# Optimization experiments

Measured on AMD Instinct MI355X. Metric: run time of the kernel, lower is better.

## Reference

```python
import jax, jax.numpy as jnp
import numpy as np

N_EMBD = 1024
N_HEAD = 16
HEAD_DIM = N_EMBD // N_HEAD
SCALE = HEAD_DIM ** -0.5


def setup_inputs() -> dict:
    key = jax.random.key(0)
    ks = jax.random.split(key, 6)
    B, T = 64, 256
    s = N_EMBD ** -0.5
    return {
        "x": jax.random.normal(ks[0], (B, T, N_EMBD), dtype=jnp.float32),
        "Wq": jax.random.normal(ks[1], (N_EMBD, N_EMBD), dtype=jnp.float32) * s,
        "Wk": jax.random.normal(ks[2], (N_EMBD, N_EMBD), dtype=jnp.float32) * s,
        "Wv": jax.random.normal(ks[3], (N_EMBD, N_EMBD), dtype=jnp.float32) * s,
        "Wo": jax.random.normal(ks[4], (N_EMBD, N_EMBD), dtype=jnp.float32) * s,
        "bo": jax.random.normal(ks[5], (N_EMBD,), dtype=jnp.float32) * 0.01,
    }


def reference(x, Wq, Wk, Wv, Wo, bo):
    B, T, C = x.shape
    # QKV projections (no bias), split heads -> [B, H, T, Dh]
    def heads(y):
        return y.reshape(B, T, N_HEAD, HEAD_DIM).transpose(0, 2, 1, 3)
    q = heads(x @ Wq)
    k = heads(x @ Wk)
    v = heads(x @ Wv)
    # scaled causal attention scores [B, H, T, T]
    wei = jnp.einsum("bhqd,bhkd->bhqk", q, k) * SCALE
    causal = jnp.tril(jnp.ones((T, T), dtype=bool))
    wei = jnp.where(causal, wei, -jnp.inf)
    wei = jax.nn.softmax(wei, axis=-1)
    # dropout is identity in eval mode
    out = jnp.einsum("bhqk,bhkd->bhqd", wei, v)
    out = out.transpose(0, 2, 1, 3).reshape(B, T, C)
    return out @ Wo + bo
```

## Files before the change

kernel.cpp:

```cpp
#include <hip/hip_runtime.h>
#include <hip/hip_bf16.h>
#include <stdint.h>

typedef __attribute__((ext_vector_type(8))) short bfx8;
typedef __attribute__((ext_vector_type(4))) short bfx4;
typedef __attribute__((ext_vector_type(4))) float f32x4;
typedef __attribute__((ext_vector_type(4))) unsigned short us4;

#define SCALE_ATT 0.125f

__device__ __forceinline__ unsigned short f2bf(float f) {
  union { float f; unsigned u; } a; a.f = f;
  unsigned r = a.u + 0x7fffu + ((a.u >> 16) & 1u);
  return (unsigned short)(r >> 16);
}

__device__ __forceinline__ void gll16(const void* g, void* l) {
  __builtin_amdgcn_global_load_lds(
      (__attribute__((address_space(1))) void*)(g),
      (__attribute__((address_space(3))) void*)(l), 16, 0, 0);
}

__device__ __forceinline__ bfx8 ld2x64(const unsigned short* p) {
  bfx4 lo = *(const bfx4*)p;
  bfx4 hi = *(const bfx4*)(p + 4);
  return __builtin_shufflevector(lo, hi, 0, 1, 2, 3, 4, 5, 6, 7);
}

__global__ __launch_bounds__(256) void cvt_x(const float* __restrict__ x,
                                             unsigned short* __restrict__ xb, int n4) {
  int i = blockIdx.x * blockDim.x + threadIdx.x;
  int stride = gridDim.x * blockDim.x;
  const float4* x4 = (const float4*)x;
  for (; i < n4; i += stride) {
    float4 v = x4[i];
    us4 o;
    o[0] = f2bf(v.x); o[1] = f2bf(v.y); o[2] = f2bf(v.z); o[3] = f2bf(v.w);
    *(us4*)&xb[(size_t)i * 4] = o;
  }
}

__global__ __launch_bounds__(256) void cvt_w(const float* __restrict__ W0, const float* __restrict__ W1,
                                             const float* __restrict__ W2, const float* __restrict__ W3,
                                             unsigned short* __restrict__ T0, unsigned short* __restrict__ T1,
                                             unsigned short* __restrict__ T2, unsigned short* __restrict__ T3) {
  const float* W; unsigned short* T;
  switch (blockIdx.z) {
    case 0: W = W0; T = T0; break;
    case 1: W = W1; T = T1; break;
    case 2: W = W2; T = T2; break;
    default: W = W3; T = T3; break;
  }
  __shared__ unsigned short Ts[64][68];
  int k0 = blockIdx.x * 64, n0 = blockIdx.y * 64;
  int t = threadIdx.x;
  int lrow = t >> 4, c4 = t & 15;
  #pragma unroll
  for (int i = 0; i < 4; i++) {
    int row = lrow + i * 16;
    float4 v = *(const float4*)&W[(size_t)(k0 + row) * 1024 + n0 + c4 * 4];
    Ts[c4 * 4 + 0][row] = f2bf(v.x);
    Ts[c4 * 4 + 1][row] = f2bf(v.y);
    Ts[c4 * 4 + 2][row] = f2bf(v.z);
    Ts[c4 * 4 + 3][row] = f2bf(v.w);
  }
  __syncthreads();
  #pragma unroll
  for (int i = 0; i < 4; i++) {
    int nrow = lrow + i * 16;
    us4 v = *(const us4*)&Ts[nrow][c4 * 4];
    *(us4*)&T[(size_t)(n0 + nrow) * 1024 + k0 + c4 * 4] = v;
  }
}

#define DS_BAR() __builtin_amdgcn_s_barrier()
#define LGKM0() do { asm volatile("s_waitcnt lgkmcnt(0)" ::: "memory"); \
                     __builtin_amdgcn_sched_barrier(0); } while (0)
#define VMW4() asm volatile("s_waitcnt vmcnt(4)" ::: "memory")
#define VMW0() asm volatile("s_waitcnt vmcnt(0)" ::: "memory")

#define STAGE(hs, gb, r0, kbyte) do { \
  const char* _g = (const char*)(gb) + (size_t)((r0) + srow) * 2048 + (size_t)(kbyte) + scolb; \
  gll16(_g, (hs) + w * 1024); \
  gll16(_g + 16 * 2048, (hs) + w * 1024 + 512); \
} while (0)

#define LOADA(dst, hs, qm) \
  _Pragma("unroll") for (int mi = 0; mi < 4; ++mi) \
    dst[mi] = *(const bfx8*)&(hs)[(wm * 128 + (qm) * 64 + mi * 16 + lr) * 32 + rcol];

#define LOADB(dst, hs) \
  _Pragma("unroll") for (int ni = 0; ni < 4; ++ni) \
    dst[ni] = *(const bfx8*)&(hs)[(wn * 64 + ni * 16 + lr) * 32 + rcol];

#define MFMA16(rb, a, b) \
  _Pragma("unroll") for (int mi = 0; mi < 4; ++mi) \
    _Pragma("unroll") for (int ni = 0; ni < 4; ++ni) \
      acc[(rb) + mi][ni] = __builtin_amdgcn_mfma_f32_16x16x32_bf16(a[mi], b[ni], acc[(rb) + mi][ni], 0, 0, 0);

#define TILE_FULL(CB, NB, KB) do {                                            \
                                                     \
    LOADA(af, A0s[CB], 0);                                                    \
    LOADB(bf0, B0s[CB]);                                                      \
    STAGE(A0s[NB], A, am0, KB);                                               \
    DS_BAR(); LGKM0();                                                        \
    __builtin_amdgcn_s_setprio(1);  MFMA16(0, af, bf0);                       \
    __builtin_amdgcn_s_setprio(0);                                            \
    DS_BAR();                                                                 \
                                                     \
    LOADA(af, A0s[CB], 1);                                                    \
    STAGE(B0s[NB], Bt, n0, KB);                                               \
    DS_BAR(); LGKM0();                                                        \
    __builtin_amdgcn_s_setprio(1);  MFMA16(4, af, bf0);                       \
    __builtin_amdgcn_s_setprio(0);                                            \
    VMW4();                                                                   \
    DS_BAR();                                                                 \
                                                     \
    LOADA(af, A1s[CB], 0);                                                    \
    LOADB(bf1, B1s[CB]);                                                      \
    STAGE(A1s[NB], A, am0, (KB) + 64);                                        \
    DS_BAR(); LGKM0();                                                        \
    __builtin_amdgcn_s_setprio(1);  MFMA16(0, af, bf1);                       \
    __builtin_amdgcn_s_setprio(0);                                            \
    DS_BAR();                                                                 \
                                                     \
    LOADA(af, A1s[CB], 1);                                                    \
    STAGE(B1s[NB], Bt, n0, (KB) + 64);                                        \
    DS_BAR(); LGKM0();                                                        \
    __builtin_amdgcn_s_setprio(1);  MFMA16(4, af, bf1);                       \
    __builtin_amdgcn_s_setprio(0);                                            \
    VMW4();                                                                   \
    DS_BAR();                                                                 \
  } while (0)

template<int MODE>
__global__ __launch_bounds__(512, 2) void gemm8p(
    const unsigned short* __restrict__ A,
    const unsigned short* __restrict__ Bt0, const unsigned short* __restrict__ Bt1,
    const unsigned short* __restrict__ Bt2,
    unsigned short* __restrict__ O0, unsigned short* __restrict__ O1,
    unsigned short* __restrict__ O2,
    const float* __restrict__ bias, float* __restrict__ OutF, int nby) {
  __shared__ unsigned short A0s[2][256 * 32];
  __shared__ unsigned short B0s[2][256 * 32];
  __shared__ unsigned short A1s[2][256 * 32];
  __shared__ unsigned short B1s[2][256 * 32];

  int tid = threadIdx.x;
  int w = tid >> 6, l = tid & 63;
  int lr = l & 15, lh = l >> 4;
  int wm = w >> 2, wn = w & 3;
  int srow = w * 32 + (l >> 2);
  int scolb = ((l & 3) * 16) ^ (((l >> 5) & 1) << 5);
  int rcol = (lh * 8) ^ (((lr >> 3) & 1) << 4);

  int cpx = gridDim.x >> 3;
  int o = blockIdx.x;
  int wg = (o & 7) * cpx + (o >> 3);
  int bm = wg / nby, bn = wg % nby;

  const unsigned short* Bt;
  unsigned short* Ob = nullptr;
  int n0;
  if (MODE == 0) {
    int sel = bn >> 2;
    n0 = (bn & 3) * 256;
    Bt = sel == 0 ? Bt0 : (sel == 1 ? Bt1 : Bt2);
    Ob = sel == 0 ? O0 : (sel == 1 ? O1 : O2);
  } else {
    Bt = Bt0;
    n0 = bn * 256;
  }
  int am0 = bm * 256;

  f32x4 acc[8][4];
  #pragma unroll
  for (int i = 0; i < 8; ++i)
    #pragma unroll
    for (int jj = 0; jj < 4; ++jj) acc[i][jj] = (f32x4){0.f, 0.f, 0.f, 0.f};

  bfx8 af[4], bf0[4], bf1[4];

  STAGE(A0s[0], A, am0, 0);   __builtin_amdgcn_sched_barrier(0);
  STAGE(B0s[0], Bt, n0, 0);   __builtin_amdgcn_sched_barrier(0);
  STAGE(A1s[0], A, am0, 64);  __builtin_amdgcn_sched_barrier(0);
  STAGE(B1s[0], Bt, n0, 64);  __builtin_amdgcn_sched_barrier(0);
  VMW4();
  DS_BAR();

  #pragma unroll 1
  for (int tp = 0; tp < 7; ++tp) {
    int kb = tp * 256;
    TILE_FULL(0, 1, kb + 128);
    TILE_FULL(1, 0, kb + 256);
  }
  TILE_FULL(0, 1, 15 * 128);
  LOADA(af, A0s[1], 0);
  LOADB(bf0, B0s[1]);
  DS_BAR(); LGKM0();
  __builtin_amdgcn_s_setprio(1);  MFMA16(0, af, bf0);
  __builtin_amdgcn_s_setprio(0);
  DS_BAR();
  LOADA(af, A0s[1], 1);
  DS_BAR(); LGKM0();
  __builtin_amdgcn_s_setprio(1);  MFMA16(4, af, bf0);
  __builtin_amdgcn_s_setprio(0);
  VMW0();
  DS_BAR();
  LOADA(af, A1s[1], 0);
  LOADB(bf1, B1s[1]);
  DS_BAR(); LGKM0();
  __builtin_amdgcn_s_setprio(1);  MFMA16(0, af, bf1);
  __builtin_amdgcn_s_setprio(0);
  DS_BAR();
  LOADA(af, A1s[1], 1);
  LGKM0();
  __builtin_amdgcn_s_setprio(1);  MFMA16(4, af, bf1);
  __builtin_amdgcn_s_setprio(0);

  float bv[4];
  if (MODE == 1) {
    #pragma unroll
    for (int ni = 0; ni < 4; ++ni) bv[ni] = bias[n0 + wn * 64 + ni * 16 + lr];
  }
  #pragma unroll
  for (int mi8 = 0; mi8 < 8; ++mi8)
    #pragma unroll
    for (int ni = 0; ni < 4; ++ni)
      #pragma unroll
      for (int j = 0; j < 4; ++j) {
        int r = am0 + wm * 128 + mi8 * 16 + lh * 4 + j;
        int c = n0 + wn * 64 + ni * 16 + lr;
        if (MODE == 0)
          Ob[(size_t)r * 1024 + c] = f2bf(acc[mi8][ni][j]);
        else
          OutF[(size_t)r * 1024 + c] = acc[mi8][ni][j] + bv[ni];
      }
}

__global__ __launch_bounds__(256) void attn_kernel(
    const unsigned short* __restrict__ Qb, const unsigned short* __restrict__ Kb,
    const unsigned short* __restrict__ Vb, unsigned short* __restrict__ Ab) {
  __shared__ unsigned short Vt[64][260];
  __shared__ unsigned short Pw[4][16][36];

  int t = threadIdx.x;
  int w = t >> 6, l = t & 63;
  int lr = l & 15, lh = l >> 4;
  int bh = blockIdx.x;
  size_t rowbase = (size_t)(bh >> 4) * 256 * 1024 + (size_t)(bh & 15) * 64;

  {
    int rr = t >> 3, part = t & 7;
    for (int i = 0; i < 8; i++) {
      int row = i * 32 + rr;
      bfx8 vv = *(const bfx8*)(Vb + rowbase + (size_t)row * 1024 + part * 8);
      #pragma unroll
      for (int e = 0; e < 8; e++) Vt[part * 8 + e][row] = (unsigned short)vv[e];
    }
  }
  __syncthreads();

  for (int qt = 0; qt < 4; qt++) {
    int r0 = qt * 64 + w * 16;
    const unsigned short* Qrow = Qb + rowbase + (size_t)(r0 + lr) * 1024 + lh * 8;
    bfx8 aq0 = *(const bfx8*)(Qrow);
    bfx8 aq1 = *(const bfx8*)(Qrow + 32);

    float m[4], lsum[4];
    #pragma unroll
    for (int j = 0; j < 4; j++) { m[j] = -1e30f; lsum[j] = 0.f; }
    f32x4 oc[4];
    #pragma unroll
    for (int ct = 0; ct < 4; ct++) oc[ct] = (f32x4){0.f, 0.f, 0.f, 0.f};

    int nkc = ((r0 + 15) >> 5) + 1;
    for (int kc = 0; kc < nkc; kc++) {
      const unsigned short* Kr = Kb + rowbase + (size_t)(kc * 32 + lr) * 1024 + lh * 8;
      bfx8 bk00 = *(const bfx8*)(Kr);
      bfx8 bk01 = *(const bfx8*)(Kr + 32);
      bfx8 bk10 = *(const bfx8*)(Kr + 16 * 1024);
      bfx8 bk11 = *(const bfx8*)(Kr + 16 * 1024 + 32);
      f32x4 s0 = (f32x4){0.f, 0.f, 0.f, 0.f};
      f32x4 s1 = (f32x4){0.f, 0.f, 0.f, 0.f};
      s0 = __builtin_amdgcn_mfma_f32_16x16x32_bf16(aq0, bk00, s0, 0, 0, 0);
      s0 = __builtin_amdgcn_mfma_f32_16x16x32_bf16(aq1, bk01, s0, 0, 0, 0);
      s1 = __builtin_amdgcn_mfma_f32_16x16x32_bf16(aq0, bk10, s1, 0, 0, 0);
      s1 = __builtin_amdgcn_mfma_f32_16x16x32_bf16(aq1, bk11, s1, 0, 0, 0);

      int c0 = kc * 32 + lr, c1 = c0 + 16;
      #pragma unroll
      for (int j = 0; j < 4; j++) {
        int row = r0 + lh * 4 + j;
        float v0 = (c0 <= row) ? s0[j] : -1e30f;
        float v1 = (c1 <= row) ? s1[j] : -1e30f;
        float cm = fmaxf(v0, v1);
        cm = fmaxf(cm, __shfl_xor(cm, 1));
        cm = fmaxf(cm, __shfl_xor(cm, 2));
        cm = fmaxf(cm, __shfl_xor(cm, 4));
        cm = fmaxf(cm, __shfl_xor(cm, 8));
        float mn = fmaxf(m[j], cm);
        float sc = __expf((m[j] - mn) * SCALE_ATT);
        float p0 = (c0 <= row) ? __expf((s0[j] - mn) * SCALE_ATT) : 0.f;
        float p1 = (c1 <= row) ? __expf((s1[j] - mn) * SCALE_ATT) : 0.f;
        m[j] = mn;
        float cs = p0 + p1;
        cs += __shfl_xor(cs, 1);
        cs += __shfl_xor(cs, 2);
        cs += __shfl_xor(cs, 4);
        cs += __shfl_xor(cs, 8);
        lsum[j] = lsum[j] * sc + cs;
        #pragma unroll
        for (int ct = 0; ct < 4; ct++) oc[ct][j] *= sc;
        Pw[w][lh * 4 + j][lr] = f2bf(p0);
        Pw[w][lh * 4 + j][16 + lr] = f2bf(p1);
      }

      bfx8 pa = ld2x64(&Pw[w][lr][lh * 8]);
      #pragma unroll
      for (int ct = 0; ct < 4; ct++) {
        bfx8 vb = ld2x64(&Vt[ct * 16 + lr][kc * 32 + lh * 8]);
        oc[ct] = __builtin_amdgcn_mfma_f32_16x16x32_bf16(pa, vb, oc[ct], 0, 0, 0);
      }
    }

    float rinv[4];
    #pragma unroll
    for (int j = 0; j < 4; j++) rinv[j] = 1.0f / lsum[j];
    #pragma unroll
    for (int ct = 0; ct < 4; ct++)
      #pragma unroll
      for (int j = 0; j < 4; j++) {
        int row = r0 + lh * 4 + j;
        Ab[rowbase + (size_t)row * 1024 + ct * 16 + lr] = f2bf(oc[ct][j] * rinv[j]);
      }
  }
}

extern "C" void kernel_launch(void* const* d_in, const int* in_sizes, int n_in,
                              void* d_out, int out_size, void* d_ws, size_t ws_size,
                              hipStream_t stream) {
  const float* x  = (const float*)d_in[0];
  const float* Wq = (const float*)d_in[1];
  const float* Wk = (const float*)d_in[2];
  const float* Wv = (const float*)d_in[3];
  const float* Wo = (const float*)d_in[4];
  const float* bo = (const float*)d_in[5];
  float* out = (float*)d_out;

  char* ws = (char*)d_ws;
  unsigned short* xb  = (unsigned short*)(ws);
  unsigned short* Wtq = (unsigned short*)(ws + (size_t)(32u << 20));
  unsigned short* Wtk = (unsigned short*)(ws + (size_t)(34u << 20));
  unsigned short* Wtv = (unsigned short*)(ws + (size_t)(36u << 20));
  unsigned short* Wto = (unsigned short*)(ws + (size_t)(38u << 20));
  unsigned short* Qb  = (unsigned short*)(ws + (size_t)(40u << 20));
  unsigned short* Kb  = (unsigned short*)(ws + (size_t)(72u << 20));
  unsigned short* Vb  = (unsigned short*)(ws + (size_t)(104u << 20));
  unsigned short* Ab  = xb;

  cvt_x<<<2048, 256, 0, stream>>>(x, xb, 4194304);
  cvt_w<<<dim3(16, 16, 4), 256, 0, stream>>>(Wq, Wk, Wv, Wo, Wtq, Wtk, Wtv, Wto);
  gemm8p<0><<<768, 512, 0, stream>>>(xb, Wtq, Wtk, Wtv, Qb, Kb, Vb, nullptr, nullptr, 12);
  attn_kernel<<<1024, 256, 0, stream>>>(Qb, Kb, Vb, Ab);
  gemm8p<1><<<256, 512, 0, stream>>>(Ab, Wto, Wto, Wto, nullptr, nullptr, nullptr, bo, out, 4);
}
```

Baseline: 243.0 us.

## Restructure GEMM main loop into halves with fewer barriers and partial LDS waits

Replaces the four-phase tile macro with a HALF macro. Each HALF reads both A quarters and the B fragment from LDS up front into separate registers. It stages A and B for the next buffer together, then waits only partially on lgkmcnt so the first MFMA batch overlaps the remaining LDS reads. This cuts the workgroup barriers per 128-wide K step from eight to two and turns the unrolled ping-pong into a rolled loop that picks buffers at runtime. It costs extra VGPRs for the second A fragment and some runtime pointer arithmetic, and it depends on the hand-tuned waitcnt values being correct.

```diff
diff --git a/kernel.cpp b/kernel.cpp
--- a/kernel.cpp
+++ b/kernel.cpp
@@ -74,7 +74,8 @@
 }
 
 #define DS_BAR() __builtin_amdgcn_s_barrier()
-#define LGKM0() do { asm volatile("s_waitcnt lgkmcnt(0)" ::: "memory"); \
+#define SB0() __builtin_amdgcn_sched_barrier(0)
+#define LGKM(N) do { asm volatile("s_waitcnt lgkmcnt(" #N ")" ::: "memory"); \
                      __builtin_amdgcn_sched_barrier(0); } while (0)
 #define VMW4() asm volatile("s_waitcnt vmcnt(4)" ::: "memory")
 #define VMW0() asm volatile("s_waitcnt vmcnt(0)" ::: "memory")
@@ -85,52 +86,32 @@
   gll16(_g + 16 * 2048, (hs) + w * 1024 + 512); \
 } while (0)
 
-#define LOADA(dst, hs, qm) \
+#define LOADA(dst, ptr, qm) \
   _Pragma("unroll") for (int mi = 0; mi < 4; ++mi) \
-    dst[mi] = *(const bfx8*)&(hs)[(wm * 128 + (qm) * 64 + mi * 16 + lr) * 32 + rcol];
-
-#define LOADB(dst, hs) \
+    dst[mi] = *(const bfx8*)&(ptr)[(wm * 128 + (qm) * 64 + mi * 16 + lr) * 32 + rcol];
+
+#define LOADB(dst, ptr) \
   _Pragma("unroll") for (int ni = 0; ni < 4; ++ni) \
-    dst[ni] = *(const bfx8*)&(hs)[(wn * 64 + ni * 16 + lr) * 32 + rcol];
+    dst[ni] = *(const bfx8*)&(ptr)[(wn * 64 + ni * 16 + lr) * 32 + rcol];
 
 #define MFMA16(rb, a, b) \
   _Pragma("unroll") for (int mi = 0; mi < 4; ++mi) \
     _Pragma("unroll") for (int ni = 0; ni < 4; ++ni) \
       acc[(rb) + mi][ni] = __builtin_amdgcn_mfma_f32_16x16x32_bf16(a[mi], b[ni], acc[(rb) + mi][ni], 0, 0, 0);
 
-#define TILE_FULL(CB, NB, KB) do {                                            \
-                                                     \
-    LOADA(af, A0s[CB], 0);                                                    \
-    LOADB(bf0, B0s[CB]);                                                      \
-    STAGE(A0s[NB], A, am0, KB);                                               \
-    DS_BAR(); LGKM0();                                                        \
-    __builtin_amdgcn_s_setprio(1);  MFMA16(0, af, bf0);                       \
+#define HALF(Ac, Bc, bfr, An, Bn, KB, STG) do {                               \
+    LOADA(af, Ac, 0);                                                         \
+    LOADB(bfr, Bc);                                                           \
+    SB0();                                                                    \
+    LOADA(ag, Ac, 1);                                                         \
+    SB0();                                                                    \
+    if (STG) { STAGE(An, A, am0, KB); STAGE(Bn, Bt, n0, KB); SB0(); }         \
+    LGKM(4);                                                                  \
+    __builtin_amdgcn_s_setprio(1);  MFMA16(0, af, bfr);                       \
     __builtin_amdgcn_s_setprio(0);                                            \
-    DS_BAR();                                                                 \
-                                                     \
-    LOADA(af, A0s[CB], 1);                                                    \
-    STAGE(B0s[NB], Bt, n0, KB);                                               \
-    DS_BAR(); LGKM0();                                                        \
-    __builtin_amdgcn_s_setprio(1);  MFMA16(4, af, bf0);                       \
+    LGKM(0);                                                                  \
+    __builtin_amdgcn_s_setprio(1);  MFMA16(4, ag, bfr);                       \
     __builtin_amdgcn_s_setprio(0);                                            \
-    VMW4();                                                                   \
-    DS_BAR();                                                                 \
-                                                     \
-    LOADA(af, A1s[CB], 0);                                                    \
-    LOADB(bf1, B1s[CB]);                                                      \
-    STAGE(A1s[NB], A, am0, (KB) + 64);                                        \
-    DS_BAR(); LGKM0();                                                        \
-    __builtin_amdgcn_s_setprio(1);  MFMA16(0, af, bf1);                       \
-    __builtin_amdgcn_s_setprio(0);                                            \
-    DS_BAR();                                                                 \
-                                                     \
-    LOADA(af, A1s[CB], 1);                                                    \
-    STAGE(B1s[NB], Bt, n0, (KB) + 64);                                        \
-    DS_BAR(); LGKM0();                                                        \
-    __builtin_amdgcn_s_setprio(1);  MFMA16(4, af, bf1);                       \
-    __builtin_amdgcn_s_setprio(0);                                            \
-    VMW4();                                                                   \
-    DS_BAR();                                                                 \
   } while (0)
 
 template<int MODE>
@@ -179,44 +160,35 @@
     #pragma unroll
     for (int jj = 0; jj < 4; ++jj) acc[i][jj] = (f32x4){0.f, 0.f, 0.f, 0.f};
 
-  bfx8 af[4], bf0[4], bf1[4];
-
-  STAGE(A0s[0], A, am0, 0);   __builtin_amdgcn_sched_barrier(0);
-  STAGE(B0s[0], Bt, n0, 0);   __builtin_amdgcn_sched_barrier(0);
-  STAGE(A1s[0], A, am0, 64);  __builtin_amdgcn_sched_barrier(0);
-  STAGE(B1s[0], Bt, n0, 64);  __builtin_amdgcn_sched_barrier(0);
+  bfx8 af[4], ag[4], bf0[4], bf1[4];
+
+  STAGE(A0s[0], A, am0, 0);   SB0();
+  STAGE(B0s[0], Bt, n0, 0);   SB0();
+  STAGE(A1s[0], A, am0, 64);  SB0();
+  STAGE(B1s[0], Bt, n0, 64);  SB0();
   VMW4();
   DS_BAR();
 
+  int cur = 0;
   #pragma unroll 1
-  for (int tp = 0; tp < 7; ++tp) {
-    int kb = tp * 256;
-    TILE_FULL(0, 1, kb + 128);
-    TILE_FULL(1, 0, kb + 256);
-  }
-  TILE_FULL(0, 1, 15 * 128);
-  LOADA(af, A0s[1], 0);
-  LOADB(bf0, B0s[1]);
-  DS_BAR(); LGKM0();
-  __builtin_amdgcn_s_setprio(1);  MFMA16(0, af, bf0);
-  __builtin_amdgcn_s_setprio(0);
-  DS_BAR();
-  LOADA(af, A0s[1], 1);
-  DS_BAR(); LGKM0();
-  __builtin_amdgcn_s_setprio(1);  MFMA16(4, af, bf0);
-  __builtin_amdgcn_s_setprio(0);
+  for (int t = 0; t < 15; ++t) {
+    int kb = (t + 1) * 128;
+    unsigned short* A0c = A0s[cur];       unsigned short* B0c = B0s[cur];
+    unsigned short* A1c = A1s[cur];       unsigned short* B1c = B1s[cur];
+    unsigned short* A0n = A0s[cur ^ 1];   unsigned short* B0n = B0s[cur ^ 1];
+    unsigned short* A1n = A1s[cur ^ 1];   unsigned short* B1n = B1s[cur ^ 1];
+    HALF(A0c, B0c, bf0, A0n, B0n, kb, 1);
+    VMW4();
+    DS_BAR();
+    HALF(A1c, B1c, bf1, A1n, B1n, kb + 64, 1);
+    VMW4();
+    DS_BAR();
+    cur ^= 1;
+  }
+  HALF(A0s[1], B0s[1], bf0, (unsigned short*)0, (unsigned short*)0, 0, 0);
   VMW0();
   DS_BAR();
-  LOADA(af, A1s[1], 0);
-  LOADB(bf1, B1s[1]);
-  DS_BAR(); LGKM0();
-  __builtin_amdgcn_s_setprio(1);  MFMA16(0, af, bf1);
-  __builtin_amdgcn_s_setprio(0);
-  DS_BAR();
-  LOADA(af, A1s[1], 1);
-  LGKM0();
-  __builtin_amdgcn_s_setprio(1);  MFMA16(4, af, bf1);
-  __builtin_amdgcn_s_setprio(0);
+  HALF(A1s[1], B1s[1], bf1, (unsigned short*)0, (unsigned short*)0, 0, 0);
 
   float bv[4];
   if (MODE == 1) {
```

After: 226.8 us. 6.7% less time.
